# Kernel tuning notes

Hardware: AMD Instinct MI355X
Metric: run time of the kernel (lower is better)

## Reference

```python
import jax, jax.numpy as jnp
import numpy as np

# Malvar-He-Cutler demosaic kernels: 4 output feature maps from the 1-channel bayer mosaic.
_K = [
    0, 0, -2, 0, 0,  0, 0, 4, 0, 0,  -2, 4, 8, 4, -2,  0, 0, 4, 0, 0,  0, 0, -2, 0, 0,
    0, 0, -3, 0, 0,  0, 4, 0, 4, 0,  -3, 0, 12, 0, -3,  0, 4, 0, 4, 0,  0, 0, -3, 0, 0,
    0, 0, 1, 0, 0,  0, -2, 0, -2, 0,  -2, 8, 10, 8, -2,  0, -2, 0, -2, 0,  0, 0, 1, 0, 0,
    0, 0, -2, 0, 0,  0, -2, 8, -2, 0,  1, 0, 10, 0, 1,  0, -2, 8, -2, 0,  0, 0, -2, 0, 0,
]
KERNELS = jnp.asarray(np.asarray(_K, dtype=np.float32).reshape(4, 1, 5, 5) / 16.0)
# Per-output-channel (R,G,B), per-quadrant (2x2) source channel into feats=(conv4 || x) -> 5 channels.
INDICES_RGGB = np.array([4, 2, 3, 1, 0, 4, 4, 0, 1, 3, 2, 4]).reshape(1, 3, 2, 2)


def _calc_index(pattern):
    p = tuple(np.asarray(pattern).flatten().tolist())
    if p == (0, 1, 1, 2):
        return INDICES_RGGB
    if p == (1, 0, 2, 1):
        return np.roll(INDICES_RGGB, 1, axis=-1)
    if p == (1, 2, 0, 1):
        return np.roll(INDICES_RGGB, 1, axis=-2)
    if p == (2, 1, 1, 0):
        return np.roll(np.roll(INDICES_RGGB, 1, axis=-1), 1, axis=-2)
    raise ValueError('Invalid bayer pattern')


def _pixel_shuffle(x, r):
    N, C, H, W = x.shape
    c = C // (r * r)
    return x.reshape(N, c, r, r, H, W).transpose(0, 1, 4, 2, 5, 3).reshape(N, c, H * r, W * r)


def _gather_bayer(x, index):
    """x: (N, C_in, H, W); index: (1|N, C_out, 2, 2) -> (N, C_out, H, W).
    Efficient equivalent of the original one-hot mask multiply-sum: a direct
    per-quadrant channel selection via take_along_axis."""
    N, C, H, W = x.shape
    iN, Cout = index.shape[0], index.shape[1]
    h, w = H // 2, W // 2
    # pixel_unshuffle(x,2) with channel order c*4 + (2*i + j): quadrant axis q.
    xq = x.reshape(N, C, h, 2, w, 2).transpose(0, 1, 3, 5, 2, 4).reshape(N, C, 4, h, w)
    xq = xq.swapaxes(1, 2)  # (N, 4, C, h, w)
    iq = index.reshape(iN, Cout, 4).swapaxes(1, 2)  # (iN, 4, Cout)
    iq = jnp.broadcast_to(iq, (N, 4, Cout))
    gath = jnp.take_along_axis(xq, iq[:, :, :, None, None], axis=2)  # (N, 4, Cout, h, w)
    y_down = gath.swapaxes(1, 2).reshape(N, Cout * 4, h, w)
    return _pixel_shuffle(y_down, 2)


def setup_inputs() -> dict:
    key = jax.random.key(0)
    x = jax.random.uniform(key, (16, 1, 1024, 1024), dtype=jnp.float32)
    bayer_pattern = jnp.array([0, 1, 1, 2], dtype=jnp.int64 if jax.config.jax_enable_x64 else jnp.int32).reshape(1, 1, 2, 2)  # RGGB
    return {"x": x, "bayer_pattern": bayer_pattern}


def reference(x, bayer_pattern) -> jnp.ndarray:
    # Replication pad by 2 on each side, then 5x5 conv producing 4 feature maps.
    x_pad = jnp.pad(x, ((0, 0), (0, 0), (2, 2), (2, 2)), mode='edge')
    feats = jax.lax.conv_general_dilated(
        x_pad, KERNELS.astype(x.dtype), window_strides=(1, 1), padding='VALID',
        dimension_numbers=('NCHW', 'OIHW', 'NCHW'))
    feats = jnp.concatenate([feats, x], axis=1)  # (N, 5, H, W)
    bp = np.asarray(bayer_pattern)  # bayer pattern is static metadata
    index = jnp.asarray(np.concatenate([_calc_index(bp[n]) for n in range(bp.shape[0])], axis=0))
    return _gather_bayer(feats, index)  # (N, 3, H, W)
```

## Files before the change

### kernel.cpp

```cpp
#include <hip/hip_runtime.h>


constexpr int H = 1024, W = 1024;

typedef float v4f  __attribute__((ext_vector_type(4)));
typedef float v4fu __attribute__((ext_vector_type(4), aligned(4)));

__global__ __launch_bounds__(256) void demosaic_kernel(
    const float* __restrict__ xin_all, const int* __restrict__ bp,
    float* __restrict__ out)
{
    const int tx  = threadIdx.x;
    const int ty  = threadIdx.y;
    const int gx  = blockIdx.x * 256 + tx * 4;
    const int ry0 = blockIdx.y * 16  + ty * 4;
    const int n   = blockIdx.z;

    const int p0 = bp[0], p1 = bp[1];
    const int fi = (p0 == 2) || (p0 == 1 && p1 == 2);
    const int fj = (p0 == 2) || (p0 == 1 && p1 == 0);

    const float* __restrict__ xin = xin_all + (size_t)n * H * W;

    const bool lfix = (gx == 0);
    const bool rfix = (gx == W - 4);
    const int  xa = lfix ? gx : gx - 2;
    const int  xb = rfix ? gx : gx + 2;

    v4f A[8], B[8];
    #pragma unroll
    for (int r = 0; r < 8; ++r) {
        const int gy = min(max(ry0 - 2 + r, 0), H - 1);
        const float* row = xin + (size_t)gy * W;
        A[r] = *(const v4fu*)(row + xa);
        B[r] = *(const v4fu*)(row + xb);
    }

    float w[8][8];
    #pragma unroll
    for (int r = 0; r < 8; ++r) {
        w[r][0] = A[r].x;
        w[r][1] = lfix ? A[r].x : A[r].y;
        w[r][2] = lfix ? A[r].x : A[r].z;
        w[r][3] = lfix ? A[r].y : A[r].w;
        w[r][4] = rfix ? B[r].z : B[r].x;
        w[r][5] = rfix ? B[r].w : B[r].y;
        w[r][6] = rfix ? B[r].w : B[r].z;
        w[r][7] = B[r].w;
    }

    #pragma unroll
    for (int dr = 0; dr < 4; ++dr) {
        const int qi = (dr & 1) ^ fi;

        float r4[4], g4[4], b4[4];
        #pragma unroll
        for (int p = 0; p < 4; ++p) {
            const float c   = w[dr + 2][p + 2];
            const float up  = w[dr + 1][p + 2], dn  = w[dr + 3][p + 2];
            const float lf  = w[dr + 2][p + 1], rt  = w[dr + 2][p + 3];
            const float up2 = w[dr + 0][p + 2], dn2 = w[dr + 4][p + 2];
            const float lf2 = w[dr + 2][p + 0], rt2 = w[dr + 2][p + 4];
            const float dg  = w[dr + 1][p + 1] + w[dr + 1][p + 3]
                            + w[dr + 3][p + 1] + w[dr + 3][p + 3];

            const float axH = lf2 + rt2;
            const float axV = up2 + dn2;
            const float ax  = axH + axV;
            const float crossHV = (up + dn) + (lf + rt);

            const float s0 = (8.0f  * c + 4.0f * crossHV   - 2.0f * ax) * 0.0625f;
            const float s1 = (12.0f * c + 4.0f * dg        - 3.0f * ax) * 0.0625f;
            const float s2 = (10.0f * c + 8.0f * (lf + rt) - 2.0f * (axH + dg) + axV) * 0.0625f;
            const float s3 = (10.0f * c + 8.0f * (up + dn) - 2.0f * (axV + dg) + axH) * 0.0625f;

            const int qj = (p & 1) ^ fj;
            const int qt = (qi << 1) | qj;
            r4[p] = (qt == 0) ? c  : (qt == 1) ? s2 : (qt == 2) ? s3 : s1;
            g4[p] = (qi == qj) ? s0 : c;
            b4[p] = (qt == 0) ? s1 : (qt == 1) ? s3 : (qt == 2) ? s2 : c;
        }

        const int y = ry0 + dr;
        const size_t rowoff = (size_t)y * W + gx;
        v4f* const oR = (v4f*)(out + (size_t)(n * 3 + 0) * H * W + rowoff);
        v4f* const oG = (v4f*)(out + (size_t)(n * 3 + 1) * H * W + rowoff);
        v4f* const oB = (v4f*)(out + (size_t)(n * 3 + 2) * H * W + rowoff);
        v4f vR = { r4[0], r4[1], r4[2], r4[3] };
        v4f vG = { g4[0], g4[1], g4[2], g4[3] };
        v4f vB = { b4[0], b4[1], b4[2], b4[3] };
        __builtin_nontemporal_store(vR, oR);
        __builtin_nontemporal_store(vG, oG);
        __builtin_nontemporal_store(vB, oB);
    }
}

extern "C" void kernel_launch(void* const* d_in, const int* in_sizes, int n_in,
                              void* d_out, int out_size, void* d_ws, size_t ws_size,
                              hipStream_t stream) {
    const float* x  = (const float*)d_in[0];
    const int*   bp = (const int*)d_in[1];
    float* out = (float*)d_out;
    const int N = in_sizes[0] / (H * W);
    dim3 grid(W / 256, H / 16, N);
    dim3 block(64, 4, 1);
    demosaic_kernel<<<grid, block, 0, stream>>>(x, bp, out);
}
```

Measured before the change: 247.3 us.

## Use persistent blocks with double-buffered register prefetch of input tiles

Replaces the one-tile-per-block grid with 512 persistent blocks, each looping over a contiguous range of tiles. While one tile is being computed, the next tile's input rows are loaded into a second register buffer, so load latency overlaps with compute and stores. This doubles the register footprint for input data, which can lower occupancy. It also assumes the tile count divides evenly by 512 and that the per-block iteration count is even; the loop would read out of bounds if it were odd.

```diff
diff --git a/kernel.cpp b/kernel.cpp
--- a/kernel.cpp
+++ b/kernel.cpp
@@ -8,90 +8,108 @@
 
 __global__ __launch_bounds__(256) void demosaic_kernel(
     const float* __restrict__ xin_all, const int* __restrict__ bp,
-    float* __restrict__ out)
+    float* __restrict__ out, int iters)
 {
     const int tx  = threadIdx.x;
     const int ty  = threadIdx.y;
-    const int gx  = blockIdx.x * 256 + tx * 4;
-    const int ry0 = blockIdx.y * 16  + ty * 4;
-    const int n   = blockIdx.z;
+    const int txo = tx * 4;
 
     const int p0 = bp[0], p1 = bp[1];
     const int fi = (p0 == 2) || (p0 == 1 && p1 == 2);
     const int fj = (p0 == 2) || (p0 == 1 && p1 == 0);
 
-    const float* __restrict__ xin = xin_all + (size_t)n * H * W;
+    auto LOADB = [&](v4f (&A)[8], v4f (&B)[8], int t) {
+        const int bx = t & 3, by = (t >> 2) & 63, n = t >> 8;
+        const int gx  = bx * 256 + txo;
+        const int ry0 = by * 16 + ty * 4;
+        const bool lf = (gx == 0), rf = (gx == W - 4);
+        const int  xa = lf ? gx : gx - 2;
+        const int  xb = rf ? gx : gx + 2;
+        const float* __restrict__ img = xin_all + (size_t)n * H * W;
+        #pragma unroll
+        for (int r = 0; r < 8; ++r) {
+            const int gy = min(max(ry0 - 2 + r, 0), H - 1);
+            const float* row = img + (size_t)gy * W;
+            A[r] = *(const v4fu*)(row + xa);
+            B[r] = *(const v4fu*)(row + xb);
+        }
+    };
 
-    const bool lfix = (gx == 0);
-    const bool rfix = (gx == W - 4);
-    const int  xa = lfix ? gx : gx - 2;
-    const int  xb = rfix ? gx : gx + 2;
+    auto PROC = [&](v4f (&A)[8], v4f (&B)[8], int t) {
+        const int bx = t & 3, by = (t >> 2) & 63, n = t >> 8;
+        const int gx  = bx * 256 + txo;
+        const int ry0 = by * 16 + ty * 4;
+        const bool lf = (gx == 0), rf = (gx == W - 4);
 
-    v4f A[8], B[8];
-    #pragma unroll
-    for (int r = 0; r < 8; ++r) {
-        const int gy = min(max(ry0 - 2 + r, 0), H - 1);
-        const float* row = xin + (size_t)gy * W;
-        A[r] = *(const v4fu*)(row + xa);
-        B[r] = *(const v4fu*)(row + xb);
-    }
-
-    float w[8][8];
-    #pragma unroll
-    for (int r = 0; r < 8; ++r) {
-        w[r][0] = A[r].x;
-        w[r][1] = lfix ? A[r].x : A[r].y;
-        w[r][2] = lfix ? A[r].x : A[r].z;
-        w[r][3] = lfix ? A[r].y : A[r].w;
-        w[r][4] = rfix ? B[r].z : B[r].x;
-        w[r][5] = rfix ? B[r].w : B[r].y;
-        w[r][6] = rfix ? B[r].w : B[r].z;
-        w[r][7] = B[r].w;
-    }
-
-    #pragma unroll
-    for (int dr = 0; dr < 4; ++dr) {
-        const int qi = (dr & 1) ^ fi;
-
-        float r4[4], g4[4], b4[4];
+        float w[8][8];
         #pragma unroll
-        for (int p = 0; p < 4; ++p) {
-            const float c   = w[dr + 2][p + 2];
-            const float up  = w[dr + 1][p + 2], dn  = w[dr + 3][p + 2];
-            const float lf  = w[dr + 2][p + 1], rt  = w[dr + 2][p + 3];
-            const float up2 = w[dr + 0][p + 2], dn2 = w[dr + 4][p + 2];
-            const float lf2 = w[dr + 2][p + 0], rt2 = w[dr + 2][p + 4];
-            const float dg  = w[dr + 1][p + 1] + w[dr + 1][p + 3]
-                            + w[dr + 3][p + 1] + w[dr + 3][p + 3];
-
-            const float axH = lf2 + rt2;
-            const float axV = up2 + dn2;
-            const float ax  = axH + axV;
-            const float crossHV = (up + dn) + (lf + rt);
-
-            const float s0 = (8.0f  * c + 4.0f * crossHV   - 2.0f * ax) * 0.0625f;
-            const float s1 = (12.0f * c + 4.0f * dg        - 3.0f * ax) * 0.0625f;
-            const float s2 = (10.0f * c + 8.0f * (lf + rt) - 2.0f * (axH + dg) + axV) * 0.0625f;
-            const float s3 = (10.0f * c + 8.0f * (up + dn) - 2.0f * (axV + dg) + axH) * 0.0625f;
-
-            const int qj = (p & 1) ^ fj;
-            const int qt = (qi << 1) | qj;
-            r4[p] = (qt == 0) ? c  : (qt == 1) ? s2 : (qt == 2) ? s3 : s1;
-            g4[p] = (qi == qj) ? s0 : c;
-            b4[p] = (qt == 0) ? s1 : (qt == 1) ? s3 : (qt == 2) ? s2 : c;
+        for (int r = 0; r < 8; ++r) {
+            w[r][0] = A[r].x;
+            w[r][1] = lf ? A[r].x : A[r].y;
+            w[r][2] = lf ? A[r].x : A[r].z;
+            w[r][3] = lf ? A[r].y : A[r].w;
+            w[r][4] = rf ? B[r].z : B[r].x;
+            w[r][5] = rf ? B[r].w : B[r].y;
+            w[r][6] = rf ? B[r].w : B[r].z;
+            w[r][7] = B[r].w;
         }
 
-        const int y = ry0 + dr;
-        const size_t rowoff = (size_t)y * W + gx;
-        v4f* const oR = (v4f*)(out + (size_t)(n * 3 + 0) * H * W + rowoff);
-        v4f* const oG = (v4f*)(out + (size_t)(n * 3 + 1) * H * W + rowoff);
-        v4f* const oB = (v4f*)(out + (size_t)(n * 3 + 2) * H * W + rowoff);
-        v4f vR = { r4[0], r4[1], r4[2], r4[3] };
-        v4f vG = { g4[0], g4[1], g4[2], g4[3] };
-        v4f vB = { b4[0], b4[1], b4[2], b4[3] };
-        __builtin_nontemporal_store(vR, oR);
-        __builtin_nontemporal_store(vG, oG);
-        __builtin_nontemporal_store(vB, oB);
+        #pragma unroll
+        for (int dr = 0; dr < 4; ++dr) {
+            const int qi = (dr & 1) ^ fi;
+
+            float r4[4], g4[4], b4[4];
+            #pragma unroll
+            for (int p = 0; p < 4; ++p) {
+                const float c   = w[dr + 2][p + 2];
+                const float up  = w[dr + 1][p + 2], dn  = w[dr + 3][p + 2];
+                const float lfv = w[dr + 2][p + 1], rt  = w[dr + 2][p + 3];
+                const float up2 = w[dr + 0][p + 2], dn2 = w[dr + 4][p + 2];
+                const float lf2 = w[dr + 2][p + 0], rt2 = w[dr + 2][p + 4];
+                const float dg  = w[dr + 1][p + 1] + w[dr + 1][p + 3]
+                                + w[dr + 3][p + 1] + w[dr + 3][p + 3];
+
+                const float axH = lf2 + rt2;
+                const float axV = up2 + dn2;
+                const float ax  = axH + axV;
+                const float crossHV = (up + dn) + (lfv + rt);
+
+                const float s0 = (8.0f  * c + 4.0f * crossHV    - 2.0f * ax) * 0.0625f;
+                const float s1 = (12.0f * c + 4.0f * dg         - 3.0f * ax) * 0.0625f;
+                const float s2 = (10.0f * c + 8.0f * (lfv + rt) - 2.0f * (axH + dg) + axV) * 0.0625f;
+                const float s3 = (10.0f * c + 8.0f * (up + dn)  - 2.0f * (axV + dg) + axH) * 0.0625f;
+
+                const int qj = (p & 1) ^ fj;
+                const int qt = (qi << 1) | qj;
+                r4[p] = (qt == 0) ? c  : (qt == 1) ? s2 : (qt == 2) ? s3 : s1;
+                g4[p] = (qi == qj) ? s0 : c;
+                b4[p] = (qt == 0) ? s1 : (qt == 1) ? s3 : (qt == 2) ? s2 : c;
+            }
+
+            const int y = ry0 + dr;
+            const size_t rowoff = (size_t)y * W + gx;
+            v4f* const oR = (v4f*)(out + (size_t)(n * 3 + 0) * H * W + rowoff);
+            v4f* const oG = (v4f*)(out + (size_t)(n * 3 + 1) * H * W + rowoff);
+            v4f* const oB = (v4f*)(out + (size_t)(n * 3 + 2) * H * W + rowoff);
+            v4f vR = { r4[0], r4[1], r4[2], r4[3] };
+            v4f vG = { g4[0], g4[1], g4[2], g4[3] };
+            v4f vB = { b4[0], b4[1], b4[2], b4[3] };
+            __builtin_nontemporal_store(vR, oR);
+            __builtin_nontemporal_store(vG, oG);
+            __builtin_nontemporal_store(vB, oB);
+        }
+    };
+
+    v4f A0[8], B0[8], A1[8], B1[8];
+    const int t0 = blockIdx.x * iters;
+
+    LOADB(A0, B0, t0);
+    #pragma unroll 1
+    for (int it = 0; it < iters; it += 2) {
+        LOADB(A1, B1, t0 + it + 1);
+        PROC(A0, B0, t0 + it);
+        if (it + 2 < iters) LOADB(A0, B0, t0 + it + 2);
+        PROC(A1, B1, t0 + it + 1);
     }
 }
 
@@ -102,7 +120,10 @@
     const int*   bp = (const int*)d_in[1];
     float* out = (float*)d_out;
     const int N = in_sizes[0] / (H * W);
-    dim3 grid(W / 256, H / 16, N);
+    const int ntiles = 4 * 64 * N;
+    const int blocks = 512;
+    const int iters  = ntiles / blocks;
+    dim3 grid(blocks, 1, 1);
     dim3 block(64, 4, 1);
-    demosaic_kernel<<<grid, block, 0, stream>>>(x, bp, out);
+    demosaic_kernel<<<grid, block, 0, stream>>>(x, bp, out, iters);
 }
```

Result: slower. 262.4 us (+6.1%).
